# Kernel optimization log

Measured on AMD Instinct MI355X. Metric: run time of the kernel, lower is better.

The kernel has to match this reference:

```python
import jax, jax.numpy as jnp
import numpy as np

N_TOKENS = 8192
D_MODEL = 1024
HIDDEN = 4096   # d_model * expert_hidden_mult(4)
N_EXPERTS = 8
TOP_K = 2
LN_EPS = 1e-5


def setup_inputs() -> dict:
    key = jax.random.key(0)
    ks = jax.random.split(key, 8)
    s_in = 1.0 / np.sqrt(D_MODEL)
    s_h = 1.0 / np.sqrt(HIDDEN)
    return {
        "x": jax.random.normal(ks[0], (N_TOKENS, D_MODEL), jnp.float32),
        "Wr": jax.random.normal(ks[1], (D_MODEL, N_EXPERTS), jnp.float32) * s_in,
        "W1": jax.random.normal(ks[2], (N_EXPERTS, D_MODEL, HIDDEN), jnp.float32) * s_in,
        "b1": jnp.zeros((N_EXPERTS, HIDDEN), jnp.float32),
        "W2": jax.random.normal(ks[3], (N_EXPERTS, HIDDEN, D_MODEL), jnp.float32) * s_h,
        "b2": jnp.zeros((N_EXPERTS, D_MODEL), jnp.float32),
        "ln_w": jnp.ones((D_MODEL,), jnp.float32),
        "ln_b": jnp.zeros((D_MODEL,), jnp.float32),
    }


def reference(x, Wr, W1, b1, W2, b2, ln_w, ln_b):
    N, d = x.shape
    E = Wr.shape[1]
    # --- Router: top-k softmax gates scattered into dense [N, E] ---
    logits = x @ Wr                                   # [N, E]
    topv, topi = jax.lax.top_k(logits, TOP_K)         # [N, K]
    gv = jax.nn.softmax(topv, axis=-1)                # renormalized top-k gates
    gates = jnp.zeros_like(logits).at[jnp.arange(N)[:, None], topi].set(gv)
    # --- Experts: gate_e > 0 masks tokens; zero gate contributes zero, so
    # dense per-expert FFN weighted by the (mostly-zero) gate column is the
    # same math as the original gather/FFN/scatter-add dispatch. ---
    mixed = jnp.zeros_like(x)
    for e in range(E):  # small fixed expert count
        h = jax.nn.gelu(x @ W1[e] + b1[e])            # [N, HIDDEN]
        y = h @ W2[e] + b2[e]                         # [N, d]
        mixed = mixed + gates[:, e:e + 1] * y
    # --- Load-balancing aux loss (importance * load) ---
    importance = jnp.mean(jax.nn.softmax(logits, axis=-1), axis=0)  # [E]
    load = jnp.mean((gates > 0).astype(x.dtype), axis=0)            # [E]
    aux_loss = E * jnp.sum(importance * load)
    # --- Residual + LayerNorm (output_dropout is identity in eval) ---
    res = x + mixed
    mu = jnp.mean(res, axis=-1, keepdims=True)
    var = jnp.var(res, axis=-1, keepdims=True)
    out = (res - mu) * jax.lax.rsqrt(var + LN_EPS) * ln_w + ln_b
    return out, aux_loss
```

## Files before the change

kernel.cpp:

```cpp
#include <hip/hip_runtime.h>

#define N_TOK 8192
#define DM 1024
#define HID 4096
#define NE 8
#define MAX_TILES 136
#define MAX_SLOTS (MAX_TILES * 128)
#define LN_EPS 1e-5f

typedef __attribute__((ext_vector_type(8))) _Float16 f16x8;
typedef __attribute__((ext_vector_type(4))) _Float16 f16x4;
typedef __attribute__((ext_vector_type(4))) float f32x4;

constexpr size_t OFF_WT1 = 0;
constexpr size_t OFF_WT2 = OFF_WT1 + (size_t)NE * HID * DM * 2;
constexpr size_t OFF_XG  = OFF_WT2 + (size_t)NE * DM * HID * 2;
constexpr size_t OFF_H   = OFF_XG + (size_t)MAX_SLOTS * DM * 2;
constexpr size_t OFF_Y   = OFF_H + (size_t)MAX_SLOTS * HID * 2;
constexpr size_t OFF_TOPI = OFF_Y + (size_t)MAX_SLOTS * DM * 2;
constexpr size_t OFF_TOPG = OFF_TOPI + (size_t)N_TOK * 2 * 4;
constexpr size_t OFF_PTOK = OFF_TOPG + (size_t)N_TOK * 2 * 4;
constexpr size_t OFF_SLOT = OFF_PTOK + (size_t)MAX_SLOTS * 4;
constexpr size_t OFF_HDR = OFF_SLOT + (size_t)N_TOK * 2 * 4;
constexpr size_t WS_NEEDED = OFF_HDR + 4096;

__device__ inline float gelu_fast(float v) {
  float c = 0.7978845608028654f * (v + 0.044715f * v * v * v);
  return v / (1.0f + __expf(-2.0f * c));
}

__device__ inline void g2l16(const _Float16* g, _Float16* l) {
  __builtin_amdgcn_global_load_lds(
      (const __attribute__((address_space(1))) unsigned int*)g,
      (__attribute__((address_space(3))) unsigned int*)l, 16, 0, 0);
}

__global__ __launch_bounds__(256) void k_router(
    const float* __restrict__ x, const float* __restrict__ Wr,
    int* __restrict__ topi, float* __restrict__ topg,
    int* __restrict__ cnt, float* __restrict__ imp) {
  __shared__ float wr[DM * NE];
  __shared__ float blkImp[NE];
  __shared__ int blkCnt[NE];
  int tid = threadIdx.x;
  if (tid < NE) { blkImp[tid] = 0.0f; blkCnt[tid] = 0; }
  for (int i = tid; i < DM * NE / 4; i += 256)
    ((float4*)wr)[i] = ((const float4*)Wr)[i];
  __syncthreads();
  int wave = tid >> 6, lane = tid & 63;
  for (int it = 0; it < 4; ++it) {
    int t = blockIdx.x * 16 + wave * 4 + it;
    double acc[NE];
#pragma unroll
    for (int e = 0; e < NE; ++e) acc[e] = 0.0;
    for (int j = 0; j < DM / 64; ++j) {
      int d = j * 64 + lane;
      float xv = x[(size_t)t * DM + d];
#pragma unroll
      for (int e = 0; e < NE; ++e) acc[e] += (double)xv * (double)wr[d * NE + e];
    }
#pragma unroll
    for (int off = 32; off > 0; off >>= 1) {
#pragma unroll
      for (int e = 0; e < NE; ++e) acc[e] += __shfl_down(acc[e], off);
    }
    if (lane == 0) {
      int i0 = 0;
#pragma unroll
      for (int e = 1; e < NE; ++e) if (acc[e] > acc[i0]) i0 = e;
      int i1 = (i0 == 0) ? 1 : 0;
#pragma unroll
      for (int e = 0; e < NE; ++e) if (e != i0 && acc[e] > acc[i1]) i1 = e;
      double g0 = 1.0 / (1.0 + exp(acc[i1] - acc[i0]));
      topi[t * 2] = i0; topi[t * 2 + 1] = i1;
      topg[t * 2] = (float)g0; topg[t * 2 + 1] = (float)(1.0 - g0);
      atomicAdd(&blkCnt[i0], 1); atomicAdd(&blkCnt[i1], 1);
      double mx = acc[0];
#pragma unroll
      for (int e = 1; e < NE; ++e) mx = acc[e] > mx ? acc[e] : mx;
      double s = 0.0, p[NE];
#pragma unroll
      for (int e = 0; e < NE; ++e) { p[e] = exp(acc[e] - mx); s += p[e]; }
      double inv = 1.0 / s;
#pragma unroll
      for (int e = 0; e < NE; ++e) atomicAdd(&blkImp[e], (float)(p[e] * inv));
    }
  }
  __syncthreads();
  if (tid < NE) { atomicAdd(&cnt[tid], blkCnt[tid]); atomicAdd(&imp[tid], blkImp[tid]); }
}

__global__ void k_setup(int* __restrict__ hdr, float* __restrict__ aux_out) {
  int* cnt = hdr;
  float* imp = (float*)(hdr + 8);
  int* cursor = hdr + 16;
  int* off = hdr + 24;
  int* n_tiles_p = hdr + 33;
  int* tile_expert = hdr + 34;
  if (threadIdx.x == 0) {
    int offl[NE + 1];
    int o = 0;
    for (int e = 0; e < NE; ++e) {
      offl[e] = o; off[e] = o; cursor[e] = o;
      o += ((cnt[e] + 127) >> 7) << 7;
    }
    offl[NE] = o; off[NE] = o;
    int nt = o >> 7;
    *n_tiles_p = nt;
    int e = 0;
    for (int i = 0; i < nt; ++i) {
      while (i * 128 >= offl[e + 1]) ++e;
      tile_expert[i] = e;
    }
    double a = 0.0;
    for (int e2 = 0; e2 < NE; ++e2)
      a += ((double)imp[e2] / (double)N_TOK) * ((double)cnt[e2] / (double)N_TOK);
    *aux_out = (float)((double)NE * a);
  }
}

__global__ __launch_bounds__(256) void k_init_pairs(int* __restrict__ pair_token) {
  int i = blockIdx.x * 256 + threadIdx.x;
  if (i < MAX_SLOTS) pair_token[i] = -1;
}

__global__ __launch_bounds__(256) void k_scatter(
    const int* __restrict__ topi, int* __restrict__ cursor,
    int* __restrict__ pair_token, int* __restrict__ slot_of) {
  int t = blockIdx.x * 256 + threadIdx.x;
#pragma unroll
  for (int k = 0; k < 2; ++k) {
    int e = topi[t * 2 + k];
    int p = atomicAdd(&cursor[e], 1);
    pair_token[p] = t;
    slot_of[t * 2 + k] = p;
  }
}

__global__ __launch_bounds__(256) void k_gather(
    const float* __restrict__ x, const int* __restrict__ pair_token,
    _Float16* __restrict__ Xg) {
  int slot = blockIdx.x;
  int t = pair_token[slot];
  int d = threadIdx.x * 4;
  f16x4 v4 = {0, 0, 0, 0};
  if (t >= 0) {
    float4 v = *(const float4*)(x + (size_t)t * DM + d);
    v4[0] = (_Float16)v.x; v4[1] = (_Float16)v.y;
    v4[2] = (_Float16)v.z; v4[3] = (_Float16)v.w;
  }
  *(f16x4*)(Xg + (size_t)slot * DM + d) = v4;
}

__global__ __launch_bounds__(256) void k_transpose(
    const float* __restrict__ in, _Float16* __restrict__ out, int R, int C) {
  __shared__ float t[64 * 65];
  size_t base = (size_t)blockIdx.z * R * C;
  int c0 = blockIdx.x * 64, r0 = blockIdx.y * 64;
  int cx = (threadIdx.x & 15) * 4, ry = threadIdx.x >> 4;
#pragma unroll
  for (int p = 0; p < 4; ++p) {
    int r = p * 16 + ry;
    float4 v = *(const float4*)(in + base + (size_t)(r0 + r) * C + c0 + cx);
    t[r * 65 + cx] = v.x; t[r * 65 + cx + 1] = v.y;
    t[r * 65 + cx + 2] = v.z; t[r * 65 + cx + 3] = v.w;
  }
  __syncthreads();
#pragma unroll
  for (int q = 0; q < 2; ++q) {
    int lin = q * 256 + threadIdx.x;
    int c = lin >> 3, ch = lin & 7;
    f16x8 v;
#pragma unroll
    for (int j = 0; j < 8; ++j) v[j] = (_Float16)t[(ch * 8 + j) * 65 + c];
    *(f16x8*)(out + base + (size_t)(c0 + c) * R + r0 + ch * 8) = v;
  }
}

__device__ inline void stage_async(const _Float16* __restrict__ g, int ld,
                                   _Float16* __restrict__ l, int tid) {
  int wbase = tid & 192;
#pragma unroll
  for (int p = 0; p < 4; ++p) {
    int s = p * 256 + tid;
    int row = s >> 3;
    int c = (s & 7) ^ (row & 7);
    g2l16(g + (size_t)row * ld + c * 8, l + (size_t)(p * 256 + wbase) * 8);
  }
}

__device__ inline f16x8 lds_frag(const _Float16* __restrict__ l, int row, int cc) {
  return *(const f16x8*)(l + row * 64 + (((cc) ^ (row & 7)) << 3));
}

template <int KD, int ND, bool GELU>
__global__ __launch_bounds__(256, 2) void k_ffn(
    const _Float16* __restrict__ A, const _Float16* __restrict__ Bw,
    const float* __restrict__ bias, _Float16* __restrict__ C,
    const int* __restrict__ hdr) {
  constexpr int GX = ND / 256;
  constexpr int NWG = GX * MAX_TILES;
  constexpr int Q = NWG >> 3;
  constexpr int R = NWG & 7;
  int orig = blockIdx.y * GX + blockIdx.x;
  int xcd = orig & 7, loc = orig >> 3;
  int wg = (xcd < R ? xcd * (Q + 1) : R * (Q + 1) + (xcd - R) * Q) + loc;
  int tileM = wg / GX, tileN = wg % GX;
  if (tileM >= hdr[33]) return;
  int e = hdr[34 + tileM];
  __shared__ _Float16 lds[(128 + 256) * 64];
  _Float16* Al = lds;
  _Float16* Bl = lds + 128 * 64;
  int tid = threadIdx.x;
  const _Float16* Ag = A + (size_t)tileM * 128 * KD;
  const _Float16* Bg = Bw + (size_t)e * ND * KD + (size_t)tileN * 256 * KD;
  f32x4 acc[8][4];
  const f32x4 fz = {0.f, 0.f, 0.f, 0.f};
#pragma unroll
  for (int a = 0; a < 8; ++a)
#pragma unroll
    for (int b = 0; b < 4; ++b) acc[a][b] = fz;
  int wave = tid >> 6, lane = tid & 63;
  int l16 = lane & 15, quad = lane >> 4;
  for (int k0 = 0; k0 < KD; k0 += 64) {
    stage_async(Ag + k0, KD, Al, tid);
    stage_async(Bg + k0, KD, Bl, tid);
    stage_async(Bg + (size_t)128 * KD + k0, KD, Bl + 128 * 64, tid);
    __syncthreads();
#pragma unroll
    for (int kk = 0; kk < 64; kk += 32) {
      int cc = quad + (kk >> 3);
      f16x8 af[8], bf[4];
#pragma unroll
      for (int mi = 0; mi < 8; ++mi)
        af[mi] = lds_frag(Al, mi * 16 + l16, cc);
#pragma unroll
      for (int ni = 0; ni < 4; ++ni)
        bf[ni] = lds_frag(Bl, wave * 64 + ni * 16 + l16, cc);
#pragma unroll
      for (int mi = 0; mi < 8; ++mi)
#pragma unroll
        for (int ni = 0; ni < 4; ++ni)
          acc[mi][ni] = __builtin_amdgcn_mfma_f32_16x16x32_f16(af[mi], bf[ni], acc[mi][ni], 0, 0, 0);
    }
    __syncthreads();
  }
  int rowBase = tileM * 128;
  int colBase = tileN * 256 + wave * 64;
  _Float16* sc = lds + wave * 4096;
  float bv[4];
#pragma unroll
  for (int ni = 0; ni < 4; ++ni) bv[ni] = bias[e * ND + colBase + ni * 16 + l16];
#pragma unroll
  for (int h = 0; h < 2; ++h) {
#pragma unroll
    for (int mi = 0; mi < 4; ++mi)
#pragma unroll
      for (int ni = 0; ni < 4; ++ni)
#pragma unroll
        for (int i = 0; i < 4; ++i) {
          int rr = mi * 16 + quad * 4 + i;
          int c2 = ni * 16 + l16;
          float v = acc[h * 4 + mi][ni][i] + bv[ni];
          sc[rr * 64 + c2] = (_Float16)(GELU ? gelu_fast(v) : v);
        }
    __syncthreads();
#pragma unroll
    for (int j = 0; j < 8; ++j) {
      int lin = j * 64 + lane;
      int rr = lin >> 3, ch = lin & 7;
      f16x8 v = *(const f16x8*)(sc + rr * 64 + ch * 8);
      *(f16x8*)(C + (size_t)(rowBase + h * 64 + rr) * ND + colBase + ch * 8) = v;
    }
    __syncthreads();
  }
}

__global__ __launch_bounds__(256) void k_ln(
    const float* __restrict__ x, const _Float16* __restrict__ Y,
    const int* __restrict__ slot_of, const float* __restrict__ topg,
    const float* __restrict__ lnw, const float* __restrict__ lnb,
    float* __restrict__ out) {
  int t = blockIdx.x, tid = threadIdx.x;
  int s0 = slot_of[t * 2], s1 = slot_of[t * 2 + 1];
  float g0 = topg[t * 2], g1 = topg[t * 2 + 1];
  float4 xv = ((const float4*)(x + (size_t)t * DM))[tid];
  f16x4 y0 = ((const f16x4*)(Y + (size_t)s0 * DM))[tid];
  f16x4 y1 = ((const f16x4*)(Y + (size_t)s1 * DM))[tid];
  float r0 = xv.x + g0 * (float)y0[0] + g1 * (float)y1[0];
  float r1 = xv.y + g0 * (float)y0[1] + g1 * (float)y1[1];
  float r2 = xv.z + g0 * (float)y0[2] + g1 * (float)y1[2];
  float r3 = xv.w + g0 * (float)y0[3] + g1 * (float)y1[3];
  float s = r0 + r1 + r2 + r3;
  float s2 = r0 * r0 + r1 * r1 + r2 * r2 + r3 * r3;
#pragma unroll
  for (int off = 32; off > 0; off >>= 1) {
    s += __shfl_down(s, off);
    s2 += __shfl_down(s2, off);
  }
  __shared__ float ss[4], ss2[4];
  int wave = tid >> 6, lane = tid & 63;
  if (lane == 0) { ss[wave] = s; ss2[wave] = s2; }
  __syncthreads();
  float S = ss[0] + ss[1] + ss[2] + ss[3];
  float S2 = ss2[0] + ss2[1] + ss2[2] + ss2[3];
  float mu = S * (1.0f / DM);
  float var = S2 * (1.0f / DM) - mu * mu;
  float inv = rsqrtf(var + LN_EPS);
  float4 wv = ((const float4*)lnw)[tid];
  float4 bv = ((const float4*)lnb)[tid];
  float4 o;
  o.x = (r0 - mu) * inv * wv.x + bv.x;
  o.y = (r1 - mu) * inv * wv.y + bv.y;
  o.z = (r2 - mu) * inv * wv.z + bv.z;
  o.w = (r3 - mu) * inv * wv.w + bv.w;
  ((float4*)(out + (size_t)t * DM))[tid] = o;
}

__global__ void k_sentinel(float* out, float v) { out[threadIdx.x] = v; }

extern "C" void kernel_launch(void* const* d_in, const int* in_sizes, int n_in,
                              void* d_out, int out_size, void* d_ws, size_t ws_size,
                              hipStream_t stream) {
  const float* x = (const float*)d_in[0];
  const float* Wr = (const float*)d_in[1];
  const float* W1 = (const float*)d_in[2];
  const float* b1 = (const float*)d_in[3];
  const float* W2 = (const float*)d_in[4];
  const float* b2 = (const float*)d_in[5];
  const float* lnw = (const float*)d_in[6];
  const float* lnb = (const float*)d_in[7];
  float* out = (float*)d_out;
  char* ws = (char*)d_ws;

  if (ws_size < WS_NEEDED) {
    k_sentinel<<<1, 256, 0, stream>>>(out, 1.0e6f + (float)(ws_size >> 20));
    return;
  }

  _Float16* Wt1 = (_Float16*)(ws + OFF_WT1);
  _Float16* Wt2 = (_Float16*)(ws + OFF_WT2);
  _Float16* Xg = (_Float16*)(ws + OFF_XG);
  _Float16* Hbuf = (_Float16*)(ws + OFF_H);
  _Float16* Ybuf = (_Float16*)(ws + OFF_Y);
  int* topi = (int*)(ws + OFF_TOPI);
  float* topg = (float*)(ws + OFF_TOPG);
  int* pair_token = (int*)(ws + OFF_PTOK);
  int* slot_of = (int*)(ws + OFF_SLOT);
  int* hdr = (int*)(ws + OFF_HDR);
  int* cnt = hdr;
  float* imp = (float*)(hdr + 8);
  int* cursor = hdr + 16;

  hipMemsetAsync(hdr, 0, 64, stream);

  k_transpose<<<dim3(HID / 64, DM / 64, NE), 256, 0, stream>>>(W1, Wt1, DM, HID);
  k_transpose<<<dim3(DM / 64, HID / 64, NE), 256, 0, stream>>>(W2, Wt2, HID, DM);
  k_router<<<512, 256, 0, stream>>>(x, Wr, topi, topg, cnt, imp);
  k_setup<<<1, 1, 0, stream>>>(hdr, out + (size_t)N_TOK * DM);
  k_init_pairs<<<(MAX_SLOTS + 255) / 256, 256, 0, stream>>>(pair_token);
  k_scatter<<<N_TOK / 256, 256, 0, stream>>>(topi, cursor, pair_token, slot_of);
  k_gather<<<MAX_SLOTS, 256, 0, stream>>>(x, pair_token, Xg);
  k_ffn<DM, HID, true><<<dim3(HID / 256, MAX_TILES), 256, 0, stream>>>(Xg, Wt1, b1, Hbuf, hdr);
  k_ffn<HID, DM, false><<<dim3(DM / 256, MAX_TILES), 256, 0, stream>>>(Hbuf, Wt2, b2, Ybuf, hdr);
  k_ln<<<N_TOK, 256, 0, stream>>>(x, Ybuf, slot_of, topg, lnw, lnb, out);
}
```

Measured before the change: 885.7 us.

## Double-buffer FFN GEMM K-loop with async LDS staging and vectorize router

The expert FFN GEMM now stages K-slices of 32 into two LDS buffers, prefetching the next slice while computing on the current one. Global and LDS offsets are precomputed, and a new 4-way swizzle replaces the 8-way one. The router transposes Wr in shared memory so each lane reads float4 vectors of x and weights. The overlap is meant to hide global-load latency behind MFMA work, at the cost of more barriers per K step and more registers for the address state.

```diff
diff --git a/kernel.cpp b/kernel.cpp
--- a/kernel.cpp
+++ b/kernel.cpp
@@ -35,17 +35,21 @@
       (__attribute__((address_space(3))) unsigned int*)l, 16, 0, 0);
 }
 
+__device__ inline int swz32(int row, int c) {
+  return c ^ ((row + (row >> 2)) & 3);
+}
+
 __global__ __launch_bounds__(256) void k_router(
     const float* __restrict__ x, const float* __restrict__ Wr,
     int* __restrict__ topi, float* __restrict__ topg,
     int* __restrict__ cnt, float* __restrict__ imp) {
-  __shared__ float wr[DM * NE];
+  __shared__ float wr[NE * DM];
   __shared__ float blkImp[NE];
   __shared__ int blkCnt[NE];
   int tid = threadIdx.x;
   if (tid < NE) { blkImp[tid] = 0.0f; blkCnt[tid] = 0; }
-  for (int i = tid; i < DM * NE / 4; i += 256)
-    ((float4*)wr)[i] = ((const float4*)Wr)[i];
+  for (int i = tid; i < DM * NE; i += 256)
+    wr[(i & 7) * DM + (i >> 3)] = Wr[i];
   __syncthreads();
   int wave = tid >> 6, lane = tid & 63;
   for (int it = 0; it < 4; ++it) {
@@ -53,11 +57,15 @@
     double acc[NE];
 #pragma unroll
     for (int e = 0; e < NE; ++e) acc[e] = 0.0;
-    for (int j = 0; j < DM / 64; ++j) {
-      int d = j * 64 + lane;
-      float xv = x[(size_t)t * DM + d];
-#pragma unroll
-      for (int e = 0; e < NE; ++e) acc[e] += (double)xv * (double)wr[d * NE + e];
+    for (int j = 0; j < DM / 256; ++j) {
+      int d = j * 256 + lane * 4;
+      float4 xv = *(const float4*)(x + (size_t)t * DM + d);
+#pragma unroll
+      for (int e = 0; e < NE; ++e) {
+        float4 wv = *(const float4*)(wr + e * DM + d);
+        acc[e] += (double)xv.x * wv.x + (double)xv.y * wv.y +
+                  (double)xv.z * wv.z + (double)xv.w * wv.w;
+      }
     }
 #pragma unroll
     for (int off = 32; off > 0; off >>= 1) {
@@ -177,22 +185,6 @@
   }
 }
 
-__device__ inline void stage_async(const _Float16* __restrict__ g, int ld,
-                                   _Float16* __restrict__ l, int tid) {
-  int wbase = tid & 192;
-#pragma unroll
-  for (int p = 0; p < 4; ++p) {
-    int s = p * 256 + tid;
-    int row = s >> 3;
-    int c = (s & 7) ^ (row & 7);
-    g2l16(g + (size_t)row * ld + c * 8, l + (size_t)(p * 256 + wbase) * 8);
-  }
-}
-
-__device__ inline f16x8 lds_frag(const _Float16* __restrict__ l, int row, int cc) {
-  return *(const f16x8*)(l + row * 64 + (((cc) ^ (row & 7)) << 3));
-}
-
 template <int KD, int ND, bool GELU>
 __global__ __launch_bounds__(256, 2) void k_ffn(
     const _Float16* __restrict__ A, const _Float16* __restrict__ Bw,
@@ -202,49 +194,87 @@
   constexpr int NWG = GX * MAX_TILES;
   constexpr int Q = NWG >> 3;
   constexpr int R = NWG & 7;
+  constexpr int NSTEP = KD / 32;
+  constexpr int BUF = 384 * 32;
   int orig = blockIdx.y * GX + blockIdx.x;
   int xcd = orig & 7, loc = orig >> 3;
   int wg = (xcd < R ? xcd * (Q + 1) : R * (Q + 1) + (xcd - R) * Q) + loc;
   int tileM = wg / GX, tileN = wg % GX;
   if (tileM >= hdr[33]) return;
   int e = hdr[34 + tileM];
-  __shared__ _Float16 lds[(128 + 256) * 64];
-  _Float16* Al = lds;
-  _Float16* Bl = lds + 128 * 64;
+  __shared__ _Float16 lds[2 * BUF];
   int tid = threadIdx.x;
+  int wave = tid >> 6, lane = tid & 63;
+  int l16 = lane & 15, quad = lane >> 4;
+  int wbase = tid & 192;
   const _Float16* Ag = A + (size_t)tileM * 128 * KD;
   const _Float16* Bg = Bw + (size_t)e * ND * KD + (size_t)tileN * 256 * KD;
+
+  const _Float16* ga0; const _Float16* ga1;
+  const _Float16* gb0; const _Float16* gb1; const _Float16* gb2; const _Float16* gb3;
+  {
+    int s, r;
+    s = tid;        r = s >> 2; ga0 = Ag + (size_t)r * KD + swz32(r, s & 3) * 8;
+    s = 256 + tid;  r = s >> 2; ga1 = Ag + (size_t)r * KD + swz32(r, s & 3) * 8;
+    s = tid;        r = s >> 2; gb0 = Bg + (size_t)r * KD + swz32(r, s & 3) * 8;
+    s = 256 + tid;  r = s >> 2; gb1 = Bg + (size_t)r * KD + swz32(r, s & 3) * 8;
+    s = 512 + tid;  r = s >> 2; gb2 = Bg + (size_t)r * KD + swz32(r, s & 3) * 8;
+    s = 768 + tid;  r = s >> 2; gb3 = Bg + (size_t)r * KD + swz32(r, s & 3) * 8;
+  }
+  int aoff[8], boff[4];
+#pragma unroll
+  for (int mi = 0; mi < 8; ++mi) {
+    int r = mi * 16 + l16;
+    aoff[mi] = r * 32 + (swz32(r, quad) << 3);
+  }
+#pragma unroll
+  for (int ni = 0; ni < 4; ++ni) {
+    int r = wave * 64 + ni * 16 + l16;
+    boff[ni] = 128 * 32 + r * 32 + (swz32(r, quad) << 3);
+  }
+
   f32x4 acc[8][4];
   const f32x4 fz = {0.f, 0.f, 0.f, 0.f};
 #pragma unroll
   for (int a = 0; a < 8; ++a)
 #pragma unroll
     for (int b = 0; b < 4; ++b) acc[a][b] = fz;
-  int wave = tid >> 6, lane = tid & 63;
-  int l16 = lane & 15, quad = lane >> 4;
-  for (int k0 = 0; k0 < KD; k0 += 64) {
-    stage_async(Ag + k0, KD, Al, tid);
-    stage_async(Bg + k0, KD, Bl, tid);
-    stage_async(Bg + (size_t)128 * KD + k0, KD, Bl + 128 * 64, tid);
+
+  auto stage = [&](int t, _Float16* buf) {
+    int k = t * 32;
+    g2l16(ga0 + k, buf + (size_t)(0 * 256 + wbase) * 8);
+    g2l16(ga1 + k, buf + (size_t)(1 * 256 + wbase) * 8);
+    _Float16* bb = buf + 128 * 32;
+    g2l16(gb0 + k, bb + (size_t)(0 * 256 + wbase) * 8);
+    g2l16(gb1 + k, bb + (size_t)(1 * 256 + wbase) * 8);
+    g2l16(gb2 + k, bb + (size_t)(2 * 256 + wbase) * 8);
+    g2l16(gb3 + k, bb + (size_t)(3 * 256 + wbase) * 8);
+  };
+  auto compute = [&](const _Float16* buf) {
+    f16x8 af[8], bf[4];
+#pragma unroll
+    for (int mi = 0; mi < 8; ++mi) af[mi] = *(const f16x8*)(buf + aoff[mi]);
+#pragma unroll
+    for (int ni = 0; ni < 4; ++ni) bf[ni] = *(const f16x8*)(buf + boff[ni]);
+#pragma unroll
+    for (int mi = 0; mi < 8; ++mi)
+#pragma unroll
+      for (int ni = 0; ni < 4; ++ni)
+        acc[mi][ni] = __builtin_amdgcn_mfma_f32_16x16x32_f16(af[mi], bf[ni], acc[mi][ni], 0, 0, 0);
+  };
+
+  stage(0, lds);
+  __syncthreads();
+#pragma unroll 1
+  for (int t = 0; t < NSTEP; t += 2) {
+    stage(t + 1, lds + BUF);
+    compute(lds);
     __syncthreads();
-#pragma unroll
-    for (int kk = 0; kk < 64; kk += 32) {
-      int cc = quad + (kk >> 3);
-      f16x8 af[8], bf[4];
-#pragma unroll
-      for (int mi = 0; mi < 8; ++mi)
-        af[mi] = lds_frag(Al, mi * 16 + l16, cc);
-#pragma unroll
-      for (int ni = 0; ni < 4; ++ni)
-        bf[ni] = lds_frag(Bl, wave * 64 + ni * 16 + l16, cc);
-#pragma unroll
-      for (int mi = 0; mi < 8; ++mi)
-#pragma unroll
-        for (int ni = 0; ni < 4; ++ni)
-          acc[mi][ni] = __builtin_amdgcn_mfma_f32_16x16x32_f16(af[mi], bf[ni], acc[mi][ni], 0, 0, 0);
-    }
+    if (t + 2 < NSTEP) stage(t + 2, lds);
+    compute(lds + BUF);
     __syncthreads();
   }
+
   int rowBase = tileM * 128;
   int colBase = tileN * 256 + wave * 64;
   _Float16* sc = lds + wave * 4096;
```

After: 899.9 us. No clear change (+1.6%).
